# Kernel optimization log

Measured on AMD Instinct MI355X. Metric: run time of the kernel, lower is better.

Reference implementation:

```python
import jax, jax.numpy as jnp
import numpy as np

DT = 0.2
N_VAR = 6
FEAT = 32


def _constants():
    dt = DT
    H = np.zeros((2, N_VAR), np.float32); H[0, 0] = 1.0; H[1, 3] = 1.0
    F = np.eye(N_VAR, dtype=np.float32)
    F[0, 1] = dt; F[0, 2] = dt * dt / 2; F[1, 2] = dt
    F[3, 4] = dt; F[3, 5] = dt * dt / 2; F[4, 5] = dt
    G = np.zeros((N_VAR, 2), np.float32)
    G[0, 0] = dt ** 3 / 6; G[1, 0] = dt * dt / 2; G[2, 0] = dt
    G[3, 1] = dt ** 3 / 6; G[4, 1] = dt * dt / 2; G[5, 1] = dt
    Bm = G.copy()  # B matrix equals G_ numerically
    return jnp.asarray(H), jnp.asarray(F), jnp.asarray(G), jnp.asarray(Bm)


def _inv2x2(S):
    a = S[..., 0, 0]; b = S[..., 0, 1]; c = S[..., 1, 0]; d = S[..., 1, 1]
    det = a * d - b * c
    inv = jnp.stack([jnp.stack([d, -b], -1), jnp.stack([-c, a], -1)], -2)
    return inv / det[..., None, None]


def _lstm(x, h, c, Wih, Whh, bih, bhh):
    gates = x @ Wih.T + bih + h @ Whh.T + bhh
    i, f, g, o = jnp.split(gates, 4, axis=-1)
    c2 = jax.nn.sigmoid(f) * c + jax.nn.sigmoid(i) * jnp.tanh(g)
    h2 = jax.nn.sigmoid(o) * jnp.tanh(c2)
    return h2, c2


def _forward(hist, position_std_x, position_std_y, velocity_std_x, velocity_std_y,
             acceleration_std_x, acceleration_std_y, jerk_std, coef_G, GR,
             cf_W, cf_b, lstm_Wih, lstm_Whh, lstm_bih, lstm_bhh, co_W, co_b, len_pred):
    H, F, G, Bm = _constants()
    Bsz = hist.shape[1]
    Z = hist[..., None]                          # (T, B, 2, 1)
    tanhG = jnp.tanh(coef_G)                     # (6,1)
    R = GR[:, None] * GR[None, :]                # (2,2)
    Gs_hist = G * tanhG * jerk_std               # (6,2)
    Q_hist = Gs_hist @ Gs_hist.T                 # (6,6)
    Id = jnp.eye(N_VAR, dtype=hist.dtype)

    # Kalman init
    V0 = (Z[1] - Z[0]) / DT                      # (B,2,1)
    X = jnp.einsum('ij,bjk->bik', H.T, Z[0])     # (B,6,1)
    X = X.at[:, 1, 0].set(V0[:, 0, 0]).at[:, 3, 0].set(V0[:, 1, 0])
    diagv = jnp.concatenate([position_std_x ** 2, velocity_std_x ** 2, acceleration_std_x ** 2,
                             position_std_y ** 2, velocity_std_y ** 2, acceleration_std_y ** 2])
    P = jnp.broadcast_to(jnp.diag(diagv), (Bsz, N_VAR, N_VAR)).astype(hist.dtype)
    h = jnp.zeros((Bsz, FEAT), hist.dtype)
    c = jnp.zeros((Bsz, FEAT), hist.dtype)

    def hist_step(carry, Zt):
        X, P, h, c = carry
        # LSTM state update (command output is discarded during history filtering)
        feat = jnp.tanh(X[:, :, 0] @ cf_W.T + cf_b)
        h, c = _lstm(feat, h, c, lstm_Wih, lstm_Whh, lstm_bih, lstm_bhh)
        # predict (no command)
        X = jnp.einsum('ij,bjk->bik', F, X)
        P = jnp.einsum('ij,bjk,lk->bil', F, P, F) + Q_hist
        # innovation
        y = Zt - jnp.einsum('ij,bjk->bik', H, X)
        S = jnp.einsum('ij,bjk,lk->bil', H, P, H) + R
        # update
        Sinv = _inv2x2(S)
        K = jnp.einsum('bij,kj,bkl->bil', P, H, Sinv)          # (B,6,2)
        X = X + K @ y
        ImKH = Id - jnp.einsum('bij,jk->bik', K, H)
        P = jnp.einsum('bij,bjk,blk->bil', ImKH, P, ImKH) + jnp.einsum('bij,jk,blk->bil', K, R, K)
        return (X, P, h, c), None

    (X, P, h, c), _ = jax.lax.scan(hist_step, (X, P, h, c), Z[1:])

    GtG = G * tanhG                                            # (6,2)

    def pred_step(carry, _):
        X, P, h, c = carry
        feat = jnp.tanh(X[:, :, 0] @ cf_W.T + cf_b)
        h, c = _lstm(feat, h, c, lstm_Wih, lstm_Whh, lstm_bih, lstm_bhh)
        command = h @ co_W.T + co_b                            # (B,4)
        X = jnp.einsum('ij,bjk->bik', F, X) + jnp.einsum('ij,bj->bi', Bm, command[:, :2])[:, :, None]
        Gs = jnp.einsum('ij,bj->bi', GtG, command[:, 2:])      # (B,6)
        Q = jnp.einsum('bi,bj->bij', Gs, Gs)
        P = jnp.einsum('ij,bjk,lk->bil', F, P, F) + Q
        mu = jnp.einsum('ij,bjk->bik', H, X)[:, :, 0]          # (B,2)
        Pout = jnp.einsum('ij,bjk,lk->bil', H, P, H)           # (B,2,2)
        return (X, P, h, c), (mu, Pout)

    _, (mu, Pout) = jax.lax.scan(pred_step, (X, P, h, c), None, length=len_pred)
    sx = jnp.sqrt(Pout[:, :, 0, 0])[..., None]
    sy = jnp.sqrt(Pout[:, :, 1, 1])[..., None]
    rho = (Pout[:, :, 0, 1] + Pout[:, :, 1, 0])[..., None] / (2 * sx * sy)
    return jnp.concatenate([mu, sx, sy, rho], axis=2)          # (len_pred, B, 5)


def setup_inputs() -> dict:
    key = jax.random.key(0)
    ks = jax.random.split(key, 8)
    T, B = 16, 32768
    u = lambda k, shape, fan: jax.random.uniform(k, shape, jnp.float32, -1.0, 1.0) / np.sqrt(fan)
    return {
        'hist': jax.random.normal(ks[0], (T, B, 2), jnp.float32),
        'position_std_x': jnp.ones((1,), jnp.float32) * 0.0519,
        'position_std_y': jnp.ones((1,), jnp.float32) * 1.7321,
        'velocity_std_x': jnp.ones((1,), jnp.float32) * 0.036,
        'velocity_std_y': jnp.ones((1,), jnp.float32) * 19.8837,
        'acceleration_std_x': jnp.ones((1,), jnp.float32) * 1e-05,
        'acceleration_std_y': jnp.ones((1,), jnp.float32) * 5.34,
        'jerk_std': jnp.array([[3.5043, 17.0283]], jnp.float32),
        'coef_G': jnp.array([[0.7427], [2.3545], [-0.0247], [-0.1391], [9.011], [0.0963]], jnp.float32),
        'GR': jnp.array([-0.0015, 0.001], jnp.float32),
        'cf_W': u(ks[1], (FEAT, N_VAR), N_VAR),
        'cf_b': u(ks[2], (FEAT,), N_VAR),
        'lstm_Wih': u(ks[3], (4 * FEAT, FEAT), FEAT),
        'lstm_Whh': u(ks[4], (4 * FEAT, FEAT), FEAT),
        'lstm_bih': u(ks[5], (4 * FEAT,), FEAT),
        'lstm_bhh': u(ks[6], (4 * FEAT,), FEAT),
        'co_W': u(ks[7], (4, FEAT), FEAT),
        'co_b': jnp.zeros((4,), jnp.float32),
        'len_pred': 25,
    }


def reference(hist, position_std_x, position_std_y, velocity_std_x, velocity_std_y,
              acceleration_std_x, acceleration_std_y, jerk_std, coef_G, GR,
              cf_W, cf_b, lstm_Wih, lstm_Whh, lstm_bih, lstm_bhh, co_W, co_b, len_pred):
    return _forward(hist, position_std_x, position_std_y, velocity_std_x, velocity_std_y,
                    acceleration_std_x, acceleration_std_y, jerk_std, coef_G, GR,
                    cf_W, cf_b, lstm_Wih, lstm_Whh, lstm_bih, lstm_bhh, co_W, co_b, int(len_pred))
```

## Files before the change

kernel.cpp:

```cpp
#include <hip/hip_runtime.h>
#include <hip/hip_bf16.h>
#include <math.h>

#define BLK 64
#define EPB 16
#define NF 32
#define THIST 15
#define CFWS 20

typedef __attribute__((ext_vector_type(8))) short s16x8;
typedef __attribute__((ext_vector_type(4))) float f32x4;

union frag_u { s16x8 v; unsigned u[4]; };

#define SWAP3216(A, B) \
    asm("v_permlane32_swap_b32 %0, %1\n\tv_permlane16_swap_b32 %0, %1" \
        : "+v"(A), "+v"(B))

__device__ __forceinline__ float frcp(float x) {
    return __builtin_amdgcn_rcpf(x);
}
__device__ __forceinline__ float sigm(float x) {
    return frcp(1.0f + __expf(-x));
}
__device__ __forceinline__ float tanhfe(float x) {
    float e = __expf(2.0f * x);
    return fmaf(-2.0f, frcp(e + 1.0f), 1.0f);
}
__device__ __forceinline__ unsigned packbf2(float x0, float x1) {
    __hip_bfloat162 b = __float22bfloat162_rn(float2{x0, x1});
    union { __hip_bfloat162 b; unsigned u; } c; c.b = b; return c.u;
}

__device__ __forceinline__ float xsum1632(float v) {
    float a = v, b = v;
    asm("v_permlane16_swap_b32 %0, %1" : "+v"(a), "+v"(b));
    float s2 = a + b;
    float p = s2, q = s2;
    asm("v_permlane32_swap_b32 %0, %1" : "+v"(p), "+v"(q));
    return p + q;
}

__device__ __forceinline__ void fpft(float (&P)[6][6]) {
    const float dt = 0.2f, hd = 0.02f;
    #pragma unroll
    for (int j = 0; j < 6; ++j) {
        float a0 = P[0][j] + dt * P[1][j] + hd * P[2][j];
        float a1 = P[1][j] + dt * P[2][j];
        float a3 = P[3][j] + dt * P[4][j] + hd * P[5][j];
        float a4 = P[4][j] + dt * P[5][j];
        P[0][j] = a0; P[1][j] = a1; P[3][j] = a3; P[4][j] = a4;
    }
    #pragma unroll
    for (int i = 0; i < 6; ++i) {
        float a0 = P[i][0] + dt * P[i][1] + hd * P[i][2];
        float a1 = P[i][1] + dt * P[i][2];
        float a3 = P[i][3] + dt * P[i][4] + hd * P[i][5];
        float a4 = P[i][4] + dt * P[i][5];
        P[i][0] = a0; P[i][1] = a1; P[i][3] = a3; P[i][4] = a4;
    }
}

__global__ __launch_bounds__(BLK, 2)
void kalman_lstm(const float* __restrict__ hist,
                 const float* __restrict__ psx, const float* __restrict__ psy,
                 const float* __restrict__ vsx, const float* __restrict__ vsy,
                 const float* __restrict__ asx, const float* __restrict__ asy,
                 const float* __restrict__ jerk, const float* __restrict__ coefG,
                 const float* __restrict__ GRv,
                 const float* __restrict__ cfW, const float* __restrict__ cfb,
                 const float* __restrict__ Wih, const float* __restrict__ Whh,
                 const float* __restrict__ bih, const float* __restrict__ bhh,
                 const float* __restrict__ coW, const float* __restrict__ cob,
                 float* __restrict__ out, int B, int len_pred)
{
    __shared__ float    cfwP[16 * CFWS];
    __shared__ float    coT[NF * 4];
    __shared__ float    kf[216];

    const int lane = threadIdx.x;
    const int e = lane & 15;
    const int s = lane >> 4;
    const int b = blockIdx.x * EPB + e;

    for (int i = lane; i < 16 * 16; i += BLK) {
        int p = i >> 4, c = i & 15;
        float v = 0.0f;
        if (c < 6)        v = cfW[(2 * p) * 6 + c];
        else if (c == 6)  v = cfb[2 * p];
        else if (c >= 8 && c < 14) v = cfW[(2 * p + 1) * 6 + (c - 8)];
        else if (c == 14) v = cfb[2 * p + 1];
        cfwP[p * CFWS + c] = v;
    }
    for (int i = lane; i < NF * 4; i += BLK) coT[i] = coW[(i & 3) * NF + (i >> 2)];

    const float dt = 0.2f, hd = 0.02f;
    const float g0 = dt * dt * dt / 6.0f, g1 = 0.02f, g2 = dt;
    float ga0 = g0 * tanhf(coefG[0]);
    float ga1 = g1 * tanhf(coefG[1]);
    float ga2 = g2 * tanhf(coefG[2]);
    float gb3 = g0 * tanhf(coefG[3]);
    float gb4 = g1 * tanhf(coefG[4]);
    float gb5 = g2 * tanhf(coefG[5]);

    {
        float j0 = jerk[0], j1 = jerk[1];
        float gr0 = GRv[0], gr1 = GRv[1];
        float R00 = gr0 * gr0, R01 = gr0 * gr1, R11 = gr1 * gr1;
        float qa[3] = {ga0 * j0, ga1 * j0, ga2 * j0};
        float qb[3] = {gb3 * j1, gb4 * j1, gb5 * j1};

        float Pk[6][6];
        #pragma unroll
        for (int i = 0; i < 6; ++i)
            #pragma unroll
            for (int j = 0; j < 6; ++j) Pk[i][j] = 0.0f;
        { float v;
          v = psx[0]; Pk[0][0] = v * v;
          v = vsx[0]; Pk[1][1] = v * v;
          v = asx[0]; Pk[2][2] = v * v;
          v = psy[0]; Pk[3][3] = v * v;
          v = vsy[0]; Pk[4][4] = v * v;
          v = asy[0]; Pk[5][5] = v * v; }

        #pragma unroll 1
        for (int t = 0; t < THIST; ++t) {
            fpft(Pk);
            #pragma unroll
            for (int i = 0; i < 3; ++i)
                #pragma unroll
                for (int j = 0; j < 3; ++j) {
                    Pk[i][j]         += qa[i] * qa[j];
                    Pk[3 + i][3 + j] += qb[i] * qb[j];
                }
            float S00 = Pk[0][0] + R00;
            float S01 = Pk[0][3] + R01;
            float S11 = Pk[3][3] + R11;
            float idet = 1.0f / (S00 * S11 - S01 * S01);
            float i00 =  S11 * idet, i01 = -S01 * idet, i11 = S00 * idet;
            float K0[6], K1[6];
            #pragma unroll
            for (int i = 0; i < 6; ++i) {
                K0[i] = Pk[i][0] * i00 + Pk[i][3] * i01;
                K1[i] = Pk[i][0] * i01 + Pk[i][3] * i11;
            }
            if (lane == 0) {
                #pragma unroll
                for (int i = 0; i < 6; ++i) {
                    kf[t * 12 + i]     = K0[i];
                    kf[t * 12 + 6 + i] = K1[i];
                }
            }
            #pragma unroll
            for (int i = 0; i < 6; ++i) {
                Pk[i][1] -= K0[1] * Pk[i][0] + K1[1] * Pk[i][3];
                Pk[i][2] -= K0[2] * Pk[i][0] + K1[2] * Pk[i][3];
                Pk[i][4] -= K0[4] * Pk[i][0] + K1[4] * Pk[i][3];
                Pk[i][5] -= K0[5] * Pk[i][0] + K1[5] * Pk[i][3];
                float t0 = Pk[i][0] - (K0[0] * Pk[i][0] + K1[0] * Pk[i][3]);
                float t3 = Pk[i][3] - (K0[3] * Pk[i][0] + K1[3] * Pk[i][3]);
                Pk[i][0] = t0; Pk[i][3] = t3;
            }
        }
        if (lane == 0) {
            #pragma unroll
            for (int i = 0; i < 6; ++i)
                #pragma unroll
                for (int j = 0; j < 6; ++j) kf[180 + i * 6 + j] = Pk[i][j];
        }
    }

    s16x8 wih_h[8], whh_h[8];
    #pragma unroll
    for (int nt = 0; nt < 8; ++nt) {
        int base = (nt * 16 + e) * NF + s * 8;
        frag_u ih_h, hh_h;
        #pragma unroll
        for (int q = 0; q < 4; ++q) {
            ih_h.u[q] = packbf2(Wih[base + 2 * q], Wih[base + 2 * q + 1]);
            hh_h.u[q] = packbf2(Whh[base + 2 * q], Whh[base + 2 * q + 1]);
        }
        wih_h[nt] = ih_h.v;
        whh_h[nt] = hh_h.v;
    }

    f32x4 biasF[8];
    #pragma unroll
    for (int nt = 0; nt < 8; ++nt) {
        int base = nt * 16 + 4 * s;
        f32x4 bi = *(const f32x4*)&bih[base];
        f32x4 bh = *(const f32x4*)&bhh[base];
        biasF[nt] = bi + bh;
    }
    float cob0 = cob[0], cob1 = cob[1], cob2 = cob[2], cob3 = cob[3];

    const float2* hist2 = (const float2*)hist;
    float2 z0 = hist2[b];
    float2 z1 = hist2[B + b];
    float X0 = z0.x, X1 = (z1.x - z0.x) / dt, X2 = 0.0f;
    float X3 = (z1.y - z0.y) / dt, X4 = 0.0f, X5 = 0.0f;

    float creg[8], hn[8];
    #pragma unroll
    for (int j = 0; j < 8; ++j) { creg[j] = 0.0f; hn[j] = 0.0f; }
    s16x8 ah_h = (s16x8)0;

    __syncthreads();

    auto lstm_step = [&]() {
        frag_u af_h;
        #pragma unroll
        for (int q = 0; q < 4; ++q) {
            int p16 = (4 * s + q) * CFWS;
            f32x4 wa = *(const f32x4*)&cfwP[p16];
            f32x4 wb = *(const f32x4*)&cfwP[p16 + 4];
            f32x4 wc = *(const f32x4*)&cfwP[p16 + 8];
            f32x4 wd = *(const f32x4*)&cfwP[p16 + 12];
            float a0 = wb[2] + wa[0] * X0 + wa[1] * X1 + wa[2] * X2
                             + wa[3] * X3 + wb[0] * X4 + wb[1] * X5;
            float a1 = wd[2] + wc[0] * X0 + wc[1] * X1 + wc[2] * X2
                             + wc[3] * X3 + wd[0] * X4 + wd[1] * X5;
            af_h.u[q] = packbf2(tanhfe(a0), tanhfe(a1));
        }

        f32x4 acc[8];
        #pragma unroll
        for (int nt = 0; nt < 8; ++nt) {
            acc[nt] = __builtin_amdgcn_mfma_f32_16x16x32_bf16(wih_h[nt], af_h.v, biasF[nt], 0, 0, 0);
            acc[nt] = __builtin_amdgcn_mfma_f32_16x16x32_bf16(whh_h[nt], ah_h, acc[nt], 0, 0, 0);
        }

        unsigned whx[2][2];
        #pragma unroll
        for (int blk = 0; blk < 2; ++blk) {
            float hv[4];
            #pragma unroll
            for (int r = 0; r < 4; ++r) {
                float gi = acc[0 + blk][r];
                float gf = acc[2 + blk][r];
                float gg = acc[4 + blk][r];
                float go = acc[6 + blk][r];
                float cn = sigm(gf) * creg[4 * blk + r] + sigm(gi) * tanhfe(gg);
                creg[4 * blk + r] = cn;
                hv[r] = sigm(go) * tanhfe(cn);
                hn[4 * blk + r] = hv[r];
            }
            #pragma unroll
            for (int rp = 0; rp < 2; ++rp)
                whx[blk][rp] = packbf2(hv[2 * rp], hv[2 * rp + 1]);
        }

        frag_u ahh;
        {
            unsigned A = whx[0][0], Bv = whx[1][0];
            SWAP3216(A, Bv); ahh.u[0] = A; ahh.u[2] = Bv;
        }
        {
            unsigned A = whx[0][1], Bv = whx[1][1];
            SWAP3216(A, Bv); ahh.u[1] = A; ahh.u[3] = Bv;
        }
        ah_h = ahh.v;
    };

    float2 zc = z1;
    #pragma unroll 1
    for (int t = 0; t < THIST; ++t) {
        int tn = (t + 2 < 16) ? (t + 2) : 15;
        float2 zn = hist2[(size_t)tn * B + b];

        lstm_step();

        f32x4 k0 = *(const f32x4*)&kf[t * 12];
        f32x4 k1 = *(const f32x4*)&kf[t * 12 + 4];
        f32x4 k2 = *(const f32x4*)&kf[t * 12 + 8];
        X0 = X0 + dt * X1 + hd * X2;  X1 = X1 + dt * X2;
        X3 = X3 + dt * X4 + hd * X5;  X4 = X4 + dt * X5;
        float y0 = zc.x - X0, y1 = zc.y - X3;
        X0 += k0[0] * y0 + k1[2] * y1;
        X1 += k0[1] * y0 + k1[3] * y1;
        X2 += k0[2] * y0 + k2[0] * y1;
        X3 += k0[3] * y0 + k2[1] * y1;
        X4 += k1[0] * y0 + k2[2] * y1;
        X5 += k1[1] * y0 + k2[3] * y1;
        zc = zn;
    }

    float xx00 = kf[180], xx01 = kf[181], xx02 = kf[182],
          xx11 = kf[187], xx12 = kf[188], xx22 = kf[194];
    float yy00 = kf[201], yy01 = kf[202], yy02 = kf[203],
          yy11 = kf[208], yy12 = kf[209], yy22 = kf[214];
    float c00 = kf[183], c01 = kf[184], c02 = kf[185],
          c10 = kf[189], c11 = kf[190], c12 = kf[191],
          c20 = kf[195], c21 = kf[196], c22 = kf[197];

    #pragma unroll 1
    for (int tp = 0; tp < len_pred; ++tp) {
        lstm_step();
        float cs0 = 0.0f, cs1 = 0.0f, cs2 = 0.0f, cs3 = 0.0f;
        #pragma unroll
        for (int blk = 0; blk < 2; ++blk)
            #pragma unroll
            for (int r = 0; r < 4; ++r) {
                int f = 16 * blk + 4 * s + r;
                f32x4 w = *(const f32x4*)&coT[f * 4];
                float hk = hn[4 * blk + r];
                cs0 += w[0] * hk;
                cs1 += w[1] * hk;
                cs2 += w[2] * hk;
                cs3 += w[3] * hk;
            }
        cs0 = xsum1632(cs0);
        cs1 = xsum1632(cs1);
        cs2 = xsum1632(cs2);
        cs3 = xsum1632(cs3);
        float cmd0 = cs0 + cob0, cmd1 = cs1 + cob1;
        float cmd2 = cs2 + cob2, cmd3 = cs3 + cob3;

        X0 = X0 + dt * X1 + hd * X2 + g0 * cmd0;
        X1 = X1 + dt * X2 + g1 * cmd0;
        X2 = X2 + g2 * cmd0;
        X3 = X3 + dt * X4 + hd * X5 + g0 * cmd1;
        X4 = X4 + dt * X5 + g1 * cmd1;
        X5 = X5 + g2 * cmd1;

        float gs0 = ga0 * cmd2, gs1 = ga1 * cmd2, gs2 = ga2 * cmd2;
        float gs3 = gb3 * cmd3, gs4 = gb4 * cmd3, gs5 = gb5 * cmd3;
        {
            float r00 = xx00 + dt * xx01 + hd * xx02;
            float r01 = xx01 + dt * xx11 + hd * xx12;
            float r02 = xx02 + dt * xx12 + hd * xx22;
            float r11 = xx11 + dt * xx12;
            float r12 = xx12 + dt * xx22;
            xx00 = r00 + dt * r01 + hd * r02;
            xx01 = r01 + dt * r02;
            xx02 = r02;
            xx11 = r11 + dt * r12;
            xx12 = r12;
            xx00 += gs0 * gs0; xx01 += gs0 * gs1; xx02 += gs0 * gs2;
            xx11 += gs1 * gs1; xx12 += gs1 * gs2; xx22 += gs2 * gs2;
        }
        {
            float r00 = yy00 + dt * yy01 + hd * yy02;
            float r01 = yy01 + dt * yy11 + hd * yy12;
            float r02 = yy02 + dt * yy12 + hd * yy22;
            float r11 = yy11 + dt * yy12;
            float r12 = yy12 + dt * yy22;
            yy00 = r00 + dt * r01 + hd * r02;
            yy01 = r01 + dt * r02;
            yy02 = r02;
            yy11 = r11 + dt * r12;
            yy12 = r12;
            yy00 += gs3 * gs3; yy01 += gs3 * gs4; yy02 += gs3 * gs5;
            yy11 += gs4 * gs4; yy12 += gs4 * gs5; yy22 += gs5 * gs5;
        }
        {
            float q00 = c00 + dt * c10 + hd * c20;
            float q01 = c01 + dt * c11 + hd * c21;
            float q02 = c02 + dt * c12 + hd * c22;
            float q10 = c10 + dt * c20;
            float q11 = c11 + dt * c21;
            float q12 = c12 + dt * c22;
            c00 = q00 + dt * q01 + hd * q02;
            c01 = q01 + dt * q02;
            c02 = q02;
            c10 = q10 + dt * q11 + hd * q12;
            c11 = q11 + dt * q12;
            c12 = q12;
            float n20 = c20 + dt * c21 + hd * c22;
            float n21 = c21 + dt * c22;
            c20 = n20; c21 = n21;
            c00 += gs0 * gs3; c01 += gs0 * gs4; c02 += gs0 * gs5;
            c10 += gs1 * gs3; c11 += gs1 * gs4; c12 += gs1 * gs5;
            c20 += gs2 * gs3; c21 += gs2 * gs4; c22 += gs2 * gs5;
        }

        float sx = sqrtf(xx00), sy = sqrtf(yy00);
        float rho = c00 / (sx * sy);
        if (s == 0) {
            size_t o = ((size_t)tp * B + b) * 5u;
            out[o + 0] = X0;
            out[o + 1] = X3;
            out[o + 2] = sx;
            out[o + 3] = sy;
            out[o + 4] = rho;
        }
    }
}

extern "C" void kernel_launch(void* const* d_in, const int* in_sizes, int n_in,
                              void* d_out, int out_size, void* d_ws, size_t ws_size,
                              hipStream_t stream) {
    const int T = 16;
    const int B = in_sizes[0] / (2 * T);
    const int len_pred = out_size / (5 * B);
    (void)d_ws; (void)ws_size; (void)n_in;

    const int grid = (B + EPB - 1) / EPB;
    kalman_lstm<<<grid, BLK, 0, stream>>>(
        (const float*)d_in[0],  (const float*)d_in[1],  (const float*)d_in[2],
        (const float*)d_in[3],  (const float*)d_in[4],  (const float*)d_in[5],
        (const float*)d_in[6],  (const float*)d_in[7],  (const float*)d_in[8],
        (const float*)d_in[9],  (const float*)d_in[10], (const float*)d_in[11],
        (const float*)d_in[12], (const float*)d_in[13], (const float*)d_in[14],
        (const float*)d_in[15], (const float*)d_in[16], (const float*)d_in[17],
        (float*)d_out, B, len_pred);
}
```

Measured before the change: 209.7 us.

## Compute feature encoder and command output with MFMA instead of scalar FMAs

Replaces the per-lane scalar state-to-feature projection and the output command dot product with bf16 MFMA instructions. The Kalman state is packed into a bf16 fragment, with a constant 1 lane carrying the bias, and fed through two MFMAs. The command uses the already-packed hidden fragment, which removes the LDS weight reads and the permlane reductions. The LSTM bias moves to LDS and is reloaded each step to free registers. The command and feature inputs now go through bf16 rounding, which may cost accuracy.

```diff
diff --git a/kernel.cpp b/kernel.cpp
--- a/kernel.cpp
+++ b/kernel.cpp
@@ -6,7 +6,6 @@
 #define EPB 16
 #define NF 32
 #define THIST 15
-#define CFWS 20
 
 typedef __attribute__((ext_vector_type(8))) short s16x8;
 typedef __attribute__((ext_vector_type(4))) float f32x4;
@@ -30,15 +29,6 @@
 __device__ __forceinline__ unsigned packbf2(float x0, float x1) {
     __hip_bfloat162 b = __float22bfloat162_rn(float2{x0, x1});
     union { __hip_bfloat162 b; unsigned u; } c; c.b = b; return c.u;
-}
-
-__device__ __forceinline__ float xsum1632(float v) {
-    float a = v, b = v;
-    asm("v_permlane16_swap_b32 %0, %1" : "+v"(a), "+v"(b));
-    float s2 = a + b;
-    float p = s2, q = s2;
-    asm("v_permlane32_swap_b32 %0, %1" : "+v"(p), "+v"(q));
-    return p + q;
 }
 
 __device__ __forceinline__ void fpft(float (&P)[6][6]) {
@@ -74,25 +64,16 @@
                  const float* __restrict__ coW, const float* __restrict__ cob,
                  float* __restrict__ out, int B, int len_pred)
 {
-    __shared__ float    cfwP[16 * CFWS];
-    __shared__ float    coT[NF * 4];
-    __shared__ float    kf[216];
+    __shared__ float biasL[128];
+    __shared__ float kf[216];
 
     const int lane = threadIdx.x;
     const int e = lane & 15;
     const int s = lane >> 4;
     const int b = blockIdx.x * EPB + e;
 
-    for (int i = lane; i < 16 * 16; i += BLK) {
-        int p = i >> 4, c = i & 15;
-        float v = 0.0f;
-        if (c < 6)        v = cfW[(2 * p) * 6 + c];
-        else if (c == 6)  v = cfb[2 * p];
-        else if (c >= 8 && c < 14) v = cfW[(2 * p + 1) * 6 + (c - 8)];
-        else if (c == 14) v = cfb[2 * p + 1];
-        cfwP[p * CFWS + c] = v;
-    }
-    for (int i = lane; i < NF * 4; i += BLK) coT[i] = coW[(i & 3) * NF + (i >> 2)];
+    biasL[lane]      = bih[lane]      + bhh[lane];
+    biasL[lane + 64] = bih[lane + 64] + bhh[lane + 64];
 
     const float dt = 0.2f, hd = 0.02f;
     const float g0 = dt * dt * dt / 6.0f, g1 = 0.02f, g2 = dt;
@@ -184,15 +165,36 @@
         whh_h[nt] = hh_h.v;
     }
 
-    f32x4 biasF[8];
-    #pragma unroll
-    for (int nt = 0; nt < 8; ++nt) {
-        int base = nt * 16 + 4 * s;
-        f32x4 bi = *(const f32x4*)&bih[base];
-        f32x4 bh = *(const f32x4*)&bhh[base];
-        biasF[nt] = bi + bh;
-    }
-    float cob0 = cob[0], cob1 = cob[1], cob2 = cob[2], cob3 = cob[3];
+    s16x8 cfwA0, cfwA1;
+    {
+        frag_u fa0, fa1; fa0.v = (s16x8)0; fa1.v = (s16x8)0;
+        if (s == 0) {
+            const float* w0 = cfW + e * 6;
+            const float* w1 = cfW + (16 + e) * 6;
+            fa0.u[0] = packbf2(w0[0], w0[1]);
+            fa0.u[1] = packbf2(w0[2], w0[3]);
+            fa0.u[2] = packbf2(w0[4], w0[5]);
+            fa0.u[3] = packbf2(cfb[e], 0.0f);
+            fa1.u[0] = packbf2(w1[0], w1[1]);
+            fa1.u[1] = packbf2(w1[2], w1[3]);
+            fa1.u[2] = packbf2(w1[4], w1[5]);
+            fa1.u[3] = packbf2(cfb[16 + e], 0.0f);
+        }
+        cfwA0 = fa0.v; cfwA1 = fa1.v;
+    }
+    s16x8 cmdA;
+    {
+        frag_u ca;
+        const float* cp = coW + (e & 3) * NF + 8 * s;
+        #pragma unroll
+        for (int q = 0; q < 4; ++q)
+            ca.u[q] = packbf2(cp[2 * q], cp[2 * q + 1]);
+        cmdA = ca.v;
+    }
+    f32x4 cobC = {cob[0], cob[1], cob[2], cob[3]};
+
+    const unsigned m0  = (s == 0) ? 0xffffffffu : 0u;
+    const unsigned xw3 = (s == 0) ? 0x00003f80u : 0u;
 
     const float2* hist2 = (const float2*)hist;
     float2 z0 = hist2[b];
@@ -200,33 +202,37 @@
     float X0 = z0.x, X1 = (z1.x - z0.x) / dt, X2 = 0.0f;
     float X3 = (z1.y - z0.y) / dt, X4 = 0.0f, X5 = 0.0f;
 
-    float creg[8], hn[8];
+    float creg[8];
     #pragma unroll
-    for (int j = 0; j < 8; ++j) { creg[j] = 0.0f; hn[j] = 0.0f; }
+    for (int j = 0; j < 8; ++j) creg[j] = 0.0f;
     s16x8 ah_h = (s16x8)0;
 
     __syncthreads();
 
     auto lstm_step = [&]() {
-        frag_u af_h;
-        #pragma unroll
-        for (int q = 0; q < 4; ++q) {
-            int p16 = (4 * s + q) * CFWS;
-            f32x4 wa = *(const f32x4*)&cfwP[p16];
-            f32x4 wb = *(const f32x4*)&cfwP[p16 + 4];
-            f32x4 wc = *(const f32x4*)&cfwP[p16 + 8];
-            f32x4 wd = *(const f32x4*)&cfwP[p16 + 12];
-            float a0 = wb[2] + wa[0] * X0 + wa[1] * X1 + wa[2] * X2
-                             + wa[3] * X3 + wb[0] * X4 + wb[1] * X5;
-            float a1 = wd[2] + wc[0] * X0 + wc[1] * X1 + wc[2] * X2
-                             + wc[3] * X3 + wd[0] * X4 + wd[1] * X5;
-            af_h.u[q] = packbf2(tanhfe(a0), tanhfe(a1));
-        }
+        frag_u xb;
+        xb.u[0] = packbf2(X0, X1) & m0;
+        xb.u[1] = packbf2(X2, X3) & m0;
+        xb.u[2] = packbf2(X4, X5) & m0;
+        xb.u[3] = xw3;
+        const f32x4 zc4 = {0.0f, 0.0f, 0.0f, 0.0f};
+        f32x4 fp0 = __builtin_amdgcn_mfma_f32_16x16x32_bf16(cfwA0, xb.v, zc4, 0, 0, 0);
+        f32x4 fp1 = __builtin_amdgcn_mfma_f32_16x16x32_bf16(cfwA1, xb.v, zc4, 0, 0, 0);
+        unsigned F00 = packbf2(tanhfe(fp0[0]), tanhfe(fp0[1]));
+        unsigned F01 = packbf2(tanhfe(fp0[2]), tanhfe(fp0[3]));
+        unsigned F10 = packbf2(tanhfe(fp1[0]), tanhfe(fp1[1]));
+        unsigned F11 = packbf2(tanhfe(fp1[2]), tanhfe(fp1[3]));
+        frag_u af;
+        { unsigned A = F00, Bv = F10; SWAP3216(A, Bv); af.u[0] = A; af.u[2] = Bv; }
+        { unsigned A = F01, Bv = F11; SWAP3216(A, Bv); af.u[1] = A; af.u[3] = Bv; }
 
         f32x4 acc[8];
         #pragma unroll
+        for (int nt = 0; nt < 8; ++nt)
+            acc[nt] = *(const f32x4*)&biasL[nt * 16 + 4 * s];
+        #pragma unroll
         for (int nt = 0; nt < 8; ++nt) {
-            acc[nt] = __builtin_amdgcn_mfma_f32_16x16x32_bf16(wih_h[nt], af_h.v, biasF[nt], 0, 0, 0);
+            acc[nt] = __builtin_amdgcn_mfma_f32_16x16x32_bf16(wih_h[nt], af.v, acc[nt], 0, 0, 0);
             acc[nt] = __builtin_amdgcn_mfma_f32_16x16x32_bf16(whh_h[nt], ah_h, acc[nt], 0, 0, 0);
         }
 
@@ -243,7 +249,6 @@
                 float cn = sigm(gf) * creg[4 * blk + r] + sigm(gi) * tanhfe(gg);
                 creg[4 * blk + r] = cn;
                 hv[r] = sigm(go) * tanhfe(cn);
-                hn[4 * blk + r] = hv[r];
             }
             #pragma unroll
             for (int rp = 0; rp < 2; ++rp)
@@ -251,14 +256,8 @@
         }
 
         frag_u ahh;
-        {
-            unsigned A = whx[0][0], Bv = whx[1][0];
-            SWAP3216(A, Bv); ahh.u[0] = A; ahh.u[2] = Bv;
-        }
-        {
-            unsigned A = whx[0][1], Bv = whx[1][1];
-            SWAP3216(A, Bv); ahh.u[1] = A; ahh.u[3] = Bv;
-        }
+        { unsigned A = whx[0][0], Bv = whx[1][0]; SWAP3216(A, Bv); ahh.u[0] = A; ahh.u[2] = Bv; }
+        { unsigned A = whx[0][1], Bv = whx[1][1]; SWAP3216(A, Bv); ahh.u[1] = A; ahh.u[3] = Bv; }
         ah_h = ahh.v;
     };
 
@@ -296,25 +295,9 @@
     #pragma unroll 1
     for (int tp = 0; tp < len_pred; ++tp) {
         lstm_step();
-        float cs0 = 0.0f, cs1 = 0.0f, cs2 = 0.0f, cs3 = 0.0f;
-        #pragma unroll
-        for (int blk = 0; blk < 2; ++blk)
-            #pragma unroll
-            for (int r = 0; r < 4; ++r) {
-                int f = 16 * blk + 4 * s + r;
-                f32x4 w = *(const f32x4*)&coT[f * 4];
-                float hk = hn[4 * blk + r];
-                cs0 += w[0] * hk;
-                cs1 += w[1] * hk;
-                cs2 += w[2] * hk;
-                cs3 += w[3] * hk;
-            }
-        cs0 = xsum1632(cs0);
-        cs1 = xsum1632(cs1);
-        cs2 = xsum1632(cs2);
-        cs3 = xsum1632(cs3);
-        float cmd0 = cs0 + cob0, cmd1 = cs1 + cob1;
-        float cmd2 = cs2 + cob2, cmd3 = cs3 + cob3;
+
+        f32x4 cm = __builtin_amdgcn_mfma_f32_16x16x32_bf16(cmdA, ah_h, cobC, 0, 0, 0);
+        float cmd0 = cm[0], cmd1 = cm[1], cmd2 = cm[2], cmd3 = cm[3];
 
         X0 = X0 + dt * X1 + hd * X2 + g0 * cmd0;
         X1 = X1 + dt * X2 + g1 * cmd0;
```

Result: faster. 199.8 us (-4.7%).
